# Kernel optimization log

Measured on AMD Instinct MI355X. Metric: run time of the kernel, lower is better.

## Reference

```python
import jax, jax.numpy as jnp
import numpy as np

B, T, D = 128, 32, 1024
ADA, INTER, RANK = 1024, 1024, 8
LN_EPS = 1e-5

def setup_inputs() -> dict:
    key = jax.random.key(0)
    ks = jax.random.split(key, 9)
    return {
        "x": jax.random.normal(ks[0], (B, T, D), dtype=jnp.float32),
        "ada_emb": jax.random.normal(ks[1], (B, ADA), dtype=jnp.float32),
        "base_layer": jax.random.normal(ks[2], (D, D), dtype=jnp.float32),  # torch.randn init
        "w1": jax.random.normal(ks[3], (ADA, INTER), dtype=jnp.float32) * 0.02,
        "b1": jnp.zeros((INTER,), dtype=jnp.float32),
        "w2": jax.random.normal(ks[4], (INTER, 2 * D * RANK), dtype=jnp.float32) * 0.02,
        "b2": jnp.zeros((2 * D * RANK,), dtype=jnp.float32),
        "ln_g": jnp.ones((ADA,), dtype=jnp.float32),
        "ln_b": jnp.zeros((ADA,), dtype=jnp.float32),
    }

def _layernorm(x, g, b):
    mu = jnp.mean(x, axis=-1, keepdims=True)
    var = jnp.var(x, axis=-1, keepdims=True)
    return (x - mu) * jax.lax.rsqrt(var + LN_EPS) * g + b

def reference(x, ada_emb, base_layer, w1, b1, w2, b2, ln_g, ln_b):
    b, t, d = x.shape
    # hypernetwork: cond -> per-sample LoRA factors
    ae = _layernorm(ada_emb, ln_g, ln_b)
    h = jax.nn.gelu(ae @ w1 + b1, approximate=False)  # nn.GELU is exact (erf)
    xw = h @ w2 + b2                                   # (B, 2*D*rank)
    x_a, x_b = jnp.split(xw, 2, axis=-1)
    x_a = x_a.reshape(b, d, RANK)
    x_b = x_b.reshape(b, d, RANK)
    # fused per-sample weight: base + x_a @ x_b^T  -> (B, D, D)
    layer = base_layer[None, :, :] + jnp.einsum('bdr,bkr->bdk', x_a, x_b)
    # apply shared per-sample weight to every token (equiv to repeat_interleave + bmm)
    out = jnp.einsum('btc,bco->bto', x, layer)
    return x + out  # residual=True
```

## Files before the change

kernel.cpp:

```cpp
#include <hip/hip_runtime.h>
#include <hip/hip_bf16.h>
#include <math.h>

#define BB    128
#define TT    32
#define DD    1024
#define NADA  1024
#define NINT  1024
#define NRANK 8
#define LNEPS 1e-5f
#define TKCH  8
#define SPL2  4
#define SPLW  2
#define XWN   (2 * DD * NRANK)

using bf16x8 = __attribute__((ext_vector_type(8))) short;
using f32x4  = __attribute__((ext_vector_type(4))) float;

__device__ __forceinline__ short f2bf(float f) {
    __hip_bfloat16 h = __float2bfloat16(f);
    return *reinterpret_cast<short*>(&h);
}

__device__ __forceinline__ void async16(const void* g, void* l) {
    __builtin_amdgcn_global_load_lds(
        (const __attribute__((address_space(1))) void*)g,
        (__attribute__((address_space(3))) void*)l, 16, 0, 0);
}

__device__ __forceinline__ void tcast_tile(
    const float* __restrict__ in, short* __restrict__ out, int K, int N,
    int bx, int by, bool addI, int tid, float (*t)[68])
{
    const int n0 = bx * 64, k0 = by * 64;
    #pragma unroll
    for (int it = 0; it < 4; ++it) {
        const int idx = it * 256 + tid;
        const int r = idx >> 4, c4 = (idx & 15) * 4;
        float4 v = *(const float4*)(in + (size_t)(k0 + r) * N + n0 + c4);
        t[r][c4 + 0] = v.x; t[r][c4 + 1] = v.y;
        t[r][c4 + 2] = v.z; t[r][c4 + 3] = v.w;
    }
    __syncthreads();
    #pragma unroll
    for (int it = 0; it < 4; ++it) {
        const int idx = it * 256 + tid;
        const int rn = idx >> 4, c4 = (idx & 15) * 4;
        float f0 = t[c4 + 0][rn], f1 = t[c4 + 1][rn];
        float f2 = t[c4 + 2][rn], f3 = t[c4 + 3][rn];
        if (addI) {
            const int n = n0 + rn;
            if (k0 + c4 + 0 == n) f0 += 1.f;
            if (k0 + c4 + 1 == n) f1 += 1.f;
            if (k0 + c4 + 2 == n) f2 += 1.f;
            if (k0 + c4 + 3 == n) f3 += 1.f;
        }
        short4 p;
        p.x = f2bf(f0); p.y = f2bf(f1); p.z = f2bf(f2); p.w = f2bf(f3);
        *(short4*)(out + (size_t)(n0 + rn) * K + k0 + c4) = p;
    }
}

__global__ __launch_bounds__(256) void prep_kernel(
    const float* __restrict__ x, const float* __restrict__ w1,
    const float* __restrict__ base, const float* __restrict__ ada,
    const float* __restrict__ lng, const float* __restrict__ lnb,
    short* __restrict__ x_bf, short* __restrict__ w1t,
    short* __restrict__ baset, short* __restrict__ ae_bf)
{
    __shared__ float t[64][68];
    const int bid = blockIdx.x, tid = threadIdx.x;

    if (bid < 2048) {
        const int i0 = bid * 512 + tid;
        float4 v0 = reinterpret_cast<const float4*>(x)[i0];
        float4 v1 = reinterpret_cast<const float4*>(x)[i0 + 256];
        short4 p0, p1;
        p0.x = f2bf(v0.x); p0.y = f2bf(v0.y); p0.z = f2bf(v0.z); p0.w = f2bf(v0.w);
        p1.x = f2bf(v1.x); p1.y = f2bf(v1.y); p1.z = f2bf(v1.z); p1.w = f2bf(v1.w);
        reinterpret_cast<short4*>(x_bf)[i0] = p0;
        reinterpret_cast<short4*>(x_bf)[i0 + 256] = p1;
    } else if (bid < 2304) {
        const int b = bid - 2048;
        tcast_tile(w1, w1t, NADA, NINT, b & 15, b >> 4, false, tid, t);
    } else if (bid < 2560) {
        const int b = bid - 2304;
        tcast_tile(base, baset, DD, DD, b & 15, b >> 4, true, tid, t);
    } else {
        const int b = bid - 2560;
        const float* row = ada + (size_t)b * NADA;
        float sum = 0.f, sumsq = 0.f;
        for (int i = tid; i < NADA; i += 256) {
            float v = row[i];
            sum += v; sumsq += v * v;
        }
        #pragma unroll
        for (int off = 32; off > 0; off >>= 1) {
            sum   += __shfl_down(sum, off);
            sumsq += __shfl_down(sumsq, off);
        }
        float* s1 = &t[0][0];
        float* s2 = &t[1][0];
        const int wid = tid >> 6, lane = tid & 63;
        if (lane == 0) { s1[wid] = sum; s2[wid] = sumsq; }
        __syncthreads();
        if (tid == 0) {
            float a = 0.f, c = 0.f;
            for (int i = 0; i < 4; ++i) { a += s1[i]; c += s2[i]; }
            s1[0] = a; s2[0] = c;
        }
        __syncthreads();
        const float mu  = s1[0] * (1.f / NADA);
        const float var = s2[0] * (1.f / NADA) - mu * mu;
        const float inv = rsqrtf(var + LNEPS);
        for (int i = tid; i < NADA; i += 256) {
            ae_bf[(size_t)b * NADA + i] = f2bf((row[i] - mu) * inv * lng[i] + lnb[i]);
        }
    }
}

template <int BM, int BN, int WM, int WN, int EPI>
__global__ __launch_bounds__(256, 2) void mgemm(
    const short* __restrict__ A, const short* __restrict__ Bt,
    float* __restrict__ C, int M, int N, int K, int kLen,
    const float* __restrict__ tp, const float* __restrict__ p3,
    const float* __restrict__ b2)
{
    constexpr int MT = BM / WM / 16;
    constexpr int NT = BN / WN / 16;
    constexpr int LA = BM / 64;
    constexpr int LB = BN / 64;

    __shared__ __align__(16) short As[BM * 32];
    __shared__ __align__(16) short Bs[BN * 32];
    __shared__ float tmS[(EPI == 2) ? BM * 8 : 1];
    __shared__ float xbS[(EPI == 2) ? (BM / 32) * BN * 8 : 1];

    const int bm = blockIdx.y * BM;
    const int bn = blockIdx.x * BN;
    const int kStart = blockIdx.z * kLen;
    const int tid = threadIdx.x;
    const int wave = tid >> 6, lane = tid & 63;
    const int wm0 = (wave / WN) * (BM / WM);
    const int wn0 = (wave % WN) * (BN / WN);
    const int quad = lane >> 4, r16 = lane & 15;

    if constexpr (EPI == 2) {
        float4 a = {0.f, 0.f, 0.f, 0.f};
        #pragma unroll
        for (int ch = 0; ch < TKCH; ++ch) {
            float4 v = *(const float4*)(tp + (size_t)ch * BB * TT * NRANK
                                           + (size_t)bm * 8 + tid * 4);
            a.x += v.x; a.y += v.y; a.z += v.z; a.w += v.w;
        }
        *(float4*)&tmS[tid * 4] = a;
        const int b0 = bm >> 5;
        const int grp = tid >> 6;
        const int inner = tid & 63;
        const size_t off = (size_t)(b0 + grp) * XWN + DD * NRANK + (size_t)bn * 8
                         + inner * 8;
        const int bcol = DD * NRANK + bn * 8 + inner * 8;
        float4 s0a = *(const float4*)(p3 + off);
        float4 s0b = *(const float4*)(p3 + off + 4);
        float4 s1a = *(const float4*)(p3 + (size_t)BB * XWN + off);
        float4 s1b = *(const float4*)(p3 + (size_t)BB * XWN + off + 4);
        float4 ba  = *(const float4*)(b2 + bcol);
        float4 bb  = *(const float4*)(b2 + bcol + 4);
        float4 r0 = {s0a.x + s1a.x + ba.x, s0a.y + s1a.y + ba.y,
                     s0a.z + s1a.z + ba.z, s0a.w + s1a.w + ba.w};
        float4 r1 = {s0b.x + s1b.x + bb.x, s0b.y + s1b.y + bb.y,
                     s0b.z + s1b.z + bb.z, s0b.w + s1b.w + bb.w};
        *(float4*)&xbS[grp * BN * 8 + inner * 8]     = r0;
        *(float4*)&xbS[grp * BN * 8 + inner * 8 + 4] = r1;
    }

    f32x4 acc[MT][NT] = {};

    for (int kt = 0; kt < kLen; kt += 32) {
        const int k0 = kStart + kt;
        #pragma unroll
        for (int s = 0; s < LA; ++s) {
            const int c = s * 256 + tid;
            async16(A + (size_t)(bm + (c >> 2)) * K + k0 + (c & 3) * 8, &As[c * 8]);
        }
        #pragma unroll
        for (int s = 0; s < LB; ++s) {
            const int c = s * 256 + tid;
            async16(Bt + (size_t)(bn + (c >> 2)) * K + k0 + (c & 3) * 8, &Bs[c * 8]);
        }
        __syncthreads();
        bf16x8 af[MT], bfr[NT];
        #pragma unroll
        for (int i = 0; i < MT; ++i)
            af[i] = *reinterpret_cast<const bf16x8*>(&As[(wm0 + i * 16 + r16) * 32 + quad * 8]);
        #pragma unroll
        for (int j = 0; j < NT; ++j)
            bfr[j] = *reinterpret_cast<const bf16x8*>(&Bs[(wn0 + j * 16 + r16) * 32 + quad * 8]);
        #pragma unroll
        for (int i = 0; i < MT; ++i)
            #pragma unroll
            for (int j = 0; j < NT; ++j)
                acc[i][j] = __builtin_amdgcn_mfma_f32_16x16x32_bf16(
                    af[i], bfr[j], acc[i][j], 0, 0, 0);
        __syncthreads();
    }

    if constexpr (EPI == 2) {
        float xbr[NT][8];
        #pragma unroll
        for (int i = 0; i < MT; ++i) {
            const int mlBase = wm0 + i * 16 + quad * 4;
            const int s = mlBase >> 5;
            #pragma unroll
            for (int j = 0; j < NT; ++j) {
                const int nl = wn0 + j * 16 + r16;
                #pragma unroll
                for (int rr = 0; rr < 8; ++rr)
                    xbr[j][rr] = xbS[(s * BN + nl) * 8 + rr];
            }
            #pragma unroll
            for (int r = 0; r < 4; ++r) {
                const int ml = mlBase + r;
                const int m = bm + ml;
                float t8[8];
                #pragma unroll
                for (int rr = 0; rr < 8; ++rr) t8[rr] = tmS[ml * 8 + rr];
                #pragma unroll
                for (int j = 0; j < NT; ++j) {
                    const int n = bn + wn0 + j * 16 + r16;
                    float v = acc[i][j][r];
                    #pragma unroll
                    for (int rr = 0; rr < 8; ++rr) v += t8[rr] * xbr[j][rr];
                    C[(size_t)m * N + n] = v;
                }
            }
        }
    } else {
        #pragma unroll
        for (int i = 0; i < MT; ++i) {
            #pragma unroll
            for (int r = 0; r < 4; ++r) {
                const int m = bm + wm0 + i * 16 + quad * 4 + r;
                #pragma unroll
                for (int j = 0; j < NT; ++j) {
                    const int n = bn + wn0 + j * 16 + r16;
                    C[((size_t)blockIdx.z * M + m) * N + n] = acc[i][j][r];
                }
            }
        }
    }
}

template <int SPLITK>
__global__ __launch_bounds__(256, 2) void gemm_w2(
    const short* __restrict__ A, const float* __restrict__ W,
    float* __restrict__ P, int M, int N, int K)
{
    constexpr int BM = 128, BN = 64;
    constexpr int MT = 4, NT = 2;
    __shared__ __align__(16) short As[BM * 32];
    __shared__ __align__(16) float Bf[32 * BN];

    const int bn = blockIdx.x * BN;
    const int kLen = K / SPLITK;
    const int kStart = blockIdx.z * kLen;
    const int tid = threadIdx.x;
    const int wave = tid >> 6, lane = tid & 63;
    const int wm0 = (wave >> 1) * 64;
    const int wn0 = (wave & 1) * 32;
    const int quad = lane >> 4, r16 = lane & 15;

    f32x4 acc[MT][NT] = {};

    for (int kt = 0; kt < kLen; kt += 32) {
        const int k0 = kStart + kt;
        #pragma unroll
        for (int s = 0; s < 2; ++s) {
            const int c = s * 256 + tid;
            async16(A + (size_t)(c >> 2) * K + k0 + (c & 3) * 8, &As[c * 8]);
        }
        #pragma unroll
        for (int s = 0; s < 2; ++s) {
            const int c = s * 256 + tid;
            async16(W + (size_t)(k0 + (c >> 4)) * N + bn + (c & 15) * 4, &Bf[c * 4]);
        }
        __syncthreads();
        bf16x8 af[MT], bfr[NT];
        #pragma unroll
        for (int i = 0; i < MT; ++i)
            af[i] = *reinterpret_cast<const bf16x8*>(&As[(wm0 + i * 16 + r16) * 32 + quad * 8]);
        #pragma unroll
        for (int j = 0; j < NT; ++j) {
            const int n = wn0 + j * 16 + r16;
            short tmp[8];
            #pragma unroll
            for (int t = 0; t < 8; ++t)
                tmp[t] = f2bf(Bf[(quad * 8 + t) * BN + n]);
            bfr[j] = *reinterpret_cast<const bf16x8*>(tmp);
        }
        #pragma unroll
        for (int i = 0; i < MT; ++i)
            #pragma unroll
            for (int j = 0; j < NT; ++j)
                acc[i][j] = __builtin_amdgcn_mfma_f32_16x16x32_bf16(
                    af[i], bfr[j], acc[i][j], 0, 0, 0);
        __syncthreads();
    }

    #pragma unroll
    for (int i = 0; i < MT; ++i) {
        #pragma unroll
        for (int r = 0; r < 4; ++r) {
            const int m = wm0 + i * 16 + quad * 4 + r;
            #pragma unroll
            for (int j = 0; j < NT; ++j) {
                const int n = bn + wn0 + j * 16 + r16;
                P[((size_t)blockIdx.z * M + m) * N + n] = acc[i][j][r];
            }
        }
    }
}

__global__ __launch_bounds__(256) void combine_gelu(
    const float* __restrict__ part, const float* __restrict__ b1,
    short* __restrict__ h)
{
    const int idx = blockIdx.x * 256 + threadIdx.x;
    float s = b1[idx & (NINT - 1)];
    #pragma unroll
    for (int z = 0; z < SPL2; ++z) s += part[(size_t)z * BB * NINT + idx];
    s = 0.5f * s * (1.f + erff(s * 0.70710678118654752f));
    h[idx] = f2bf(s);
}

__global__ __launch_bounds__(256) void tpart_kernel(
    const float* __restrict__ x, const float* __restrict__ p3,
    const float* __restrict__ b2, float* __restrict__ tp)
{
    __shared__ float xa[(DD / TKCH) * NRANK];
    const int b = blockIdx.x, ch = blockIdx.y;
    const int col0 = ch * (DD / TKCH) * NRANK;
    const size_t off = (size_t)b * XWN + col0;
    {
        const int i4 = threadIdx.x * 4;
        float4 v0 = *(const float4*)(p3 + off + i4);
        float4 v1 = *(const float4*)(p3 + (size_t)BB * XWN + off + i4);
        float4 vb = *(const float4*)(b2 + col0 + i4);
        float4 r = {v0.x + v1.x + vb.x, v0.y + v1.y + vb.y,
                    v0.z + v1.z + vb.z, v0.w + v1.w + vb.w};
        *(float4*)(xa + i4) = r;
    }
    __syncthreads();
    const int m = threadIdx.x >> 3;
    const int r = threadIdx.x & 7;
    const float* xrow = x + ((size_t)b * TT + m) * DD + ch * (DD / TKCH);
    float accv = 0.f;
    #pragma unroll 4
    for (int c = 0; c < DD / TKCH; c += 4) {
        float4 xr = *(const float4*)(xrow + c);
        accv += xr.x * xa[(c + 0) * NRANK + r];
        accv += xr.y * xa[(c + 1) * NRANK + r];
        accv += xr.z * xa[(c + 2) * NRANK + r];
        accv += xr.w * xa[(c + 3) * NRANK + r];
    }
    tp[((size_t)ch * BB * TT + (size_t)b * TT + m) * NRANK + r] = accv;
}

extern "C" void kernel_launch(void* const* d_in, const int* in_sizes, int n_in,
                              void* d_out, int out_size, void* d_ws, size_t ws_size,
                              hipStream_t stream)
{
    const float* x    = (const float*)d_in[0];
    const float* ada  = (const float*)d_in[1];
    const float* base = (const float*)d_in[2];
    const float* w1   = (const float*)d_in[3];
    const float* b1   = (const float*)d_in[4];
    const float* w2   = (const float*)d_in[5];
    const float* b2   = (const float*)d_in[6];
    const float* lng  = (const float*)d_in[7];
    const float* lnb  = (const float*)d_in[8];
    float* out = (float*)d_out;

    char* w = (char*)d_ws;
    short* x_bf  = (short*)w;  w += (size_t)8 << 20;
    short* w1t   = (short*)w;  w += (size_t)2 << 20;
    short* baset = (short*)w;  w += (size_t)2 << 20;
    short* ae_bf = (short*)w;  w += (size_t)256 << 10;
    short* h_bf  = (short*)w;  w += (size_t)256 << 10;
    float* p3    = (float*)w;  w += (size_t)16 << 20;
    float* tp    = (float*)w;  w += (size_t)1 << 20;
    float* part  = (float*)w;

    prep_kernel<<<2688, 256, 0, stream>>>(
        x, w1, base, ada, lng, lnb, x_bf, w1t, baset, ae_bf);
    mgemm<64, 64, 2, 2, 0><<<dim3(NINT / 64, BB / 64, SPL2), 256, 0, stream>>>(
        ae_bf, w1t, part, BB, NINT, NADA, NADA / SPL2, nullptr, nullptr, nullptr);
    combine_gelu<<<BB * NINT / 256, 256, 0, stream>>>(part, b1, h_bf);
    gemm_w2<SPLW><<<dim3(XWN / 64, 1, SPLW), 256, 0, stream>>>(
        h_bf, w2, p3, BB, XWN, NINT);
    tpart_kernel<<<dim3(BB, TKCH), 256, 0, stream>>>(x, p3, b2, tp);
    mgemm<128, 64, 2, 2, 2><<<dim3(DD / 64, BB * TT / 128), 256, 0, stream>>>(
        x_bf, baset, out, BB * TT, DD, DD, DD, tp, p3, b2);
}
```

Before: 183.1 us.

## Deepen GEMM K-steps, vectorize gelu combine, read bf16 x in tpart

```diff
diff --git a/kernel.cpp b/kernel.cpp
--- a/kernel.cpp
+++ b/kernel.cpp
@@ -10,7 +10,7 @@
 #define NRANK 8
 #define LNEPS 1e-5f
 #define TKCH  8
-#define SPL2  4
+#define SPL2  8
 #define SPLW  2
 #define XWN   (2 * DD * NRANK)
 
@@ -20,6 +20,11 @@
 __device__ __forceinline__ short f2bf(float f) {
     __hip_bfloat16 h = __float2bfloat16(f);
     return *reinterpret_cast<short*>(&h);
+}
+
+__device__ __forceinline__ float bf2f(short s) {
+    unsigned u = ((unsigned)(unsigned short)s) << 16;
+    return __uint_as_float(u);
 }
 
 __device__ __forceinline__ void async16(const void* g, void* l) {
@@ -131,8 +136,8 @@
     constexpr int LA = BM / 64;
     constexpr int LB = BN / 64;
 
-    __shared__ __align__(16) short As[BM * 32];
-    __shared__ __align__(16) short Bs[BN * 32];
+    __shared__ __align__(16) short As[BM * 64];
+    __shared__ __align__(16) short Bs[BN * 64];
     __shared__ float tmS[(EPI == 2) ? BM * 8 : 1];
     __shared__ float xbS[(EPI == 2) ? (BM / 32) * BN * 8 : 1];
 
@@ -176,32 +181,42 @@
 
     f32x4 acc[MT][NT] = {};
 
-    for (int kt = 0; kt < kLen; kt += 32) {
+    for (int kt = 0; kt < kLen; kt += 64) {
         const int k0 = kStart + kt;
         #pragma unroll
-        for (int s = 0; s < LA; ++s) {
-            const int c = s * 256 + tid;
-            async16(A + (size_t)(bm + (c >> 2)) * K + k0 + (c & 3) * 8, &As[c * 8]);
-        }
-        #pragma unroll
-        for (int s = 0; s < LB; ++s) {
-            const int c = s * 256 + tid;
-            async16(Bt + (size_t)(bn + (c >> 2)) * K + k0 + (c & 3) * 8, &Bs[c * 8]);
-        }
-        __syncthreads();
-        bf16x8 af[MT], bfr[NT];
-        #pragma unroll
-        for (int i = 0; i < MT; ++i)
-            af[i] = *reinterpret_cast<const bf16x8*>(&As[(wm0 + i * 16 + r16) * 32 + quad * 8]);
-        #pragma unroll
-        for (int j = 0; j < NT; ++j)
-            bfr[j] = *reinterpret_cast<const bf16x8*>(&Bs[(wn0 + j * 16 + r16) * 32 + quad * 8]);
-        #pragma unroll
-        for (int i = 0; i < MT; ++i)
+        for (int kk = 0; kk < 2; ++kk) {
+            #pragma unroll
+            for (int s = 0; s < LA; ++s) {
+                const int c = s * 256 + tid;
+                async16(A + (size_t)(bm + (c >> 2)) * K + k0 + kk * 32 + (c & 3) * 8,
+                        &As[kk * BM * 32 + c * 8]);
+            }
+            #pragma unroll
+            for (int s = 0; s < LB; ++s) {
+                const int c = s * 256 + tid;
+                async16(Bt + (size_t)(bn + (c >> 2)) * K + k0 + kk * 32 + (c & 3) * 8,
+                        &Bs[kk * BN * 32 + c * 8]);
+            }
+        }
+        __syncthreads();
+        #pragma unroll
+        for (int kk = 0; kk < 2; ++kk) {
+            bf16x8 af[MT], bfr[NT];
+            #pragma unroll
+            for (int i = 0; i < MT; ++i)
+                af[i] = *reinterpret_cast<const bf16x8*>(
+                    &As[kk * BM * 32 + (wm0 + i * 16 + r16) * 32 + quad * 8]);
             #pragma unroll
             for (int j = 0; j < NT; ++j)
-                acc[i][j] = __builtin_amdgcn_mfma_f32_16x16x32_bf16(
-                    af[i], bfr[j], acc[i][j], 0, 0, 0);
+                bfr[j] = *reinterpret_cast<const bf16x8*>(
+                    &Bs[kk * BN * 32 + (wn0 + j * 16 + r16) * 32 + quad * 8]);
+            #pragma unroll
+            for (int i = 0; i < MT; ++i)
+                #pragma unroll
+                for (int j = 0; j < NT; ++j)
+                    acc[i][j] = __builtin_amdgcn_mfma_f32_16x16x32_bf16(
+                        af[i], bfr[j], acc[i][j], 0, 0, 0);
+        }
         __syncthreads();
     }
 
@@ -258,8 +273,8 @@
 {
     constexpr int BM = 128, BN = 64;
     constexpr int MT = 4, NT = 2;
-    __shared__ __align__(16) short As[BM * 32];
-    __shared__ __align__(16) float Bf[32 * BN];
+    __shared__ __align__(16) short As[BM * 64];
+    __shared__ __align__(16) float Bf[64 * BN];
 
     const int bn = blockIdx.x * BN;
     const int kLen = K / SPLITK;
@@ -272,38 +287,47 @@
 
     f32x4 acc[MT][NT] = {};
 
-    for (int kt = 0; kt < kLen; kt += 32) {
+    for (int kt = 0; kt < kLen; kt += 64) {
         const int k0 = kStart + kt;
         #pragma unroll
-        for (int s = 0; s < 2; ++s) {
-            const int c = s * 256 + tid;
-            async16(A + (size_t)(c >> 2) * K + k0 + (c & 3) * 8, &As[c * 8]);
-        }
-        #pragma unroll
-        for (int s = 0; s < 2; ++s) {
-            const int c = s * 256 + tid;
-            async16(W + (size_t)(k0 + (c >> 4)) * N + bn + (c & 15) * 4, &Bf[c * 4]);
-        }
-        __syncthreads();
-        bf16x8 af[MT], bfr[NT];
-        #pragma unroll
-        for (int i = 0; i < MT; ++i)
-            af[i] = *reinterpret_cast<const bf16x8*>(&As[(wm0 + i * 16 + r16) * 32 + quad * 8]);
-        #pragma unroll
-        for (int j = 0; j < NT; ++j) {
-            const int n = wn0 + j * 16 + r16;
-            short tmp[8];
-            #pragma unroll
-            for (int t = 0; t < 8; ++t)
-                tmp[t] = f2bf(Bf[(quad * 8 + t) * BN + n]);
-            bfr[j] = *reinterpret_cast<const bf16x8*>(tmp);
-        }
-        #pragma unroll
-        for (int i = 0; i < MT; ++i)
-            #pragma unroll
-            for (int j = 0; j < NT; ++j)
-                acc[i][j] = __builtin_amdgcn_mfma_f32_16x16x32_bf16(
-                    af[i], bfr[j], acc[i][j], 0, 0, 0);
+        for (int kk = 0; kk < 2; ++kk) {
+            #pragma unroll
+            for (int s = 0; s < 2; ++s) {
+                const int c = s * 256 + tid;
+                async16(A + (size_t)(c >> 2) * K + k0 + kk * 32 + (c & 3) * 8,
+                        &As[kk * BM * 32 + c * 8]);
+            }
+            #pragma unroll
+            for (int s = 0; s < 2; ++s) {
+                const int c = s * 256 + tid;
+                async16(W + (size_t)(k0 + kk * 32 + (c >> 4)) * N + bn + (c & 15) * 4,
+                        &Bf[kk * 32 * BN + c * 4]);
+            }
+        }
+        __syncthreads();
+        #pragma unroll
+        for (int kk = 0; kk < 2; ++kk) {
+            bf16x8 af[MT], bfr[NT];
+            #pragma unroll
+            for (int i = 0; i < MT; ++i)
+                af[i] = *reinterpret_cast<const bf16x8*>(
+                    &As[kk * BM * 32 + (wm0 + i * 16 + r16) * 32 + quad * 8]);
+            #pragma unroll
+            for (int j = 0; j < NT; ++j) {
+                const int n = wn0 + j * 16 + r16;
+                short tmp[8];
+                #pragma unroll
+                for (int t = 0; t < 8; ++t)
+                    tmp[t] = f2bf(Bf[kk * 32 * BN + (quad * 8 + t) * BN + n]);
+                bfr[j] = *reinterpret_cast<const bf16x8*>(tmp);
+            }
+            #pragma unroll
+            for (int i = 0; i < MT; ++i)
+                #pragma unroll
+                for (int j = 0; j < NT; ++j)
+                    acc[i][j] = __builtin_amdgcn_mfma_f32_16x16x32_bf16(
+                        af[i], bfr[j], acc[i][j], 0, 0, 0);
+        }
         __syncthreads();
     }
 
@@ -325,16 +349,24 @@
     const float* __restrict__ part, const float* __restrict__ b1,
     short* __restrict__ h)
 {
-    const int idx = blockIdx.x * 256 + threadIdx.x;
-    float s = b1[idx & (NINT - 1)];
+    const int i4 = (blockIdx.x * 256 + threadIdx.x) * 4;
+    float4 s = *(const float4*)(b1 + (i4 & (NINT - 1)));
     #pragma unroll
-    for (int z = 0; z < SPL2; ++z) s += part[(size_t)z * BB * NINT + idx];
-    s = 0.5f * s * (1.f + erff(s * 0.70710678118654752f));
-    h[idx] = f2bf(s);
+    for (int z = 0; z < SPL2; ++z) {
+        float4 p = *(const float4*)(part + (size_t)z * BB * NINT + i4);
+        s.x += p.x; s.y += p.y; s.z += p.z; s.w += p.w;
+    }
+    s.x = 0.5f * s.x * (1.f + erff(s.x * 0.70710678118654752f));
+    s.y = 0.5f * s.y * (1.f + erff(s.y * 0.70710678118654752f));
+    s.z = 0.5f * s.z * (1.f + erff(s.z * 0.70710678118654752f));
+    s.w = 0.5f * s.w * (1.f + erff(s.w * 0.70710678118654752f));
+    short4 o;
+    o.x = f2bf(s.x); o.y = f2bf(s.y); o.z = f2bf(s.z); o.w = f2bf(s.w);
+    *(short4*)(h + i4) = o;
 }
 
 __global__ __launch_bounds__(256) void tpart_kernel(
-    const float* __restrict__ x, const float* __restrict__ p3,
+    const short* __restrict__ x_bf, const float* __restrict__ p3,
     const float* __restrict__ b2, float* __restrict__ tp)
 {
     __shared__ float xa[(DD / TKCH) * NRANK];
@@ -353,15 +385,14 @@
     __syncthreads();
     const int m = threadIdx.x >> 3;
     const int r = threadIdx.x & 7;
-    const float* xrow = x + ((size_t)b * TT + m) * DD + ch * (DD / TKCH);
+    const short* xrow = x_bf + ((size_t)b * TT + m) * DD + ch * (DD / TKCH);
     float accv = 0.f;
-    #pragma unroll 4
-    for (int c = 0; c < DD / TKCH; c += 4) {
-        float4 xr = *(const float4*)(xrow + c);
-        accv += xr.x * xa[(c + 0) * NRANK + r];
-        accv += xr.y * xa[(c + 1) * NRANK + r];
-        accv += xr.z * xa[(c + 2) * NRANK + r];
-        accv += xr.w * xa[(c + 3) * NRANK + r];
+    #pragma unroll 2
+    for (int c = 0; c < DD / TKCH; c += 8) {
+        bf16x8 xr = *(const bf16x8*)(xrow + c);
+        #pragma unroll
+        for (int u = 0; u < 8; ++u)
+            accv += bf2f(xr[u]) * xa[(c + u) * NRANK + r];
     }
     tp[((size_t)ch * BB * TT + (size_t)b * TT + m) * NRANK + r] = accv;
 }
@@ -395,10 +426,10 @@
         x, w1, base, ada, lng, lnb, x_bf, w1t, baset, ae_bf);
     mgemm<64, 64, 2, 2, 0><<<dim3(NINT / 64, BB / 64, SPL2), 256, 0, stream>>>(
         ae_bf, w1t, part, BB, NINT, NADA, NADA / SPL2, nullptr, nullptr, nullptr);
-    combine_gelu<<<BB * NINT / 256, 256, 0, stream>>>(part, b1, h_bf);
+    combine_gelu<<<BB * NINT / 1024, 256, 0, stream>>>(part, b1, h_bf);
     gemm_w2<SPLW><<<dim3(XWN / 64, 1, SPLW), 256, 0, stream>>>(
         h_bf, w2, p3, BB, XWN, NINT);
-    tpart_kernel<<<dim3(BB, TKCH), 256, 0, stream>>>(x, p3, b2, tp);
+    tpart_kernel<<<dim3(BB, TKCH), 256, 0, stream>>>(x_bf, p3, b2, tp);
     mgemm<128, 64, 2, 2, 2><<<dim3(DD / 64, BB * TT / 128), 256, 0, stream>>>(
         x_bf, baset, out, BB * TT, DD, DD, DD, tp, p3, b2);
 }
```

New measurement: 178.0 us. 2.8% less time.
